# Kernel tuning notes

Measured on AMD Instinct MI355X. Metric: run time of the kernel, lower is better.

## Reference

```python
import jax, jax.numpy as jnp
import numpy as np

B, S, DM, H, DFF, NL = 4, 1024, 512, 8, 2048, 2
D = DM // H
EPS = 1e-9


def setup_inputs() -> dict:
    key = jax.random.key(0)
    ks = jax.random.split(key, 16)
    x = jax.random.normal(ks[0], (B, S, DM), jnp.float32)
    # padding-style mask: 1.0 where attention is blocked
    pad = (jax.random.uniform(ks[1], (B, S)) < 0.1).astype(jnp.float32)
    mask = jnp.maximum(pad[:, :, None], pad[:, None, :])  # [B,S,S]
    protok = jax.random.randint(ks[2], (B, S), 0, 21).astype(jnp.int32)

    def w(k, fan_in, fan_out):
        lim = np.sqrt(6.0 / (fan_in + fan_out)).astype(np.float32)
        return jax.random.uniform(k, (fan_in, fan_out), jnp.float32, -lim, lim)

    return {
        "x": x, "mask": mask, "protok": protok,
        "wq": w(ks[3], DM, DM), "bq": jnp.zeros((DM,), jnp.float32),
        "wk": w(ks[4], DM, DM), "bk": jnp.zeros((DM,), jnp.float32),
        "wv": w(ks[5], DM, DM), "bv": jnp.zeros((DM,), jnp.float32),
        "wo": w(ks[6], DM, DM), "bo": jnp.zeros((DM,), jnp.float32),
        "w1": w(ks[7], DM, DFF), "b1": jnp.zeros((DFF,), jnp.float32),
        "w2": w(ks[8], DFF, DM), "b2": jnp.zeros((DM,), jnp.float32),
        "ln1_g": jnp.ones((DM,), jnp.float32), "ln1_b": jnp.zeros((DM,), jnp.float32),
        "ln2_g": jnp.ones((DM,), jnp.float32), "ln2_b": jnp.zeros((DM,), jnp.float32),
        "layer_num": NL,
    }


def _layernorm(y, g, b):
    m = jnp.mean(y, axis=-1, keepdims=True)
    v = jnp.mean(jnp.square(y - m), axis=-1, keepdims=True)
    return (y - m) * jax.lax.rsqrt(v + EPS) * g + b


def reference(x, mask, protok, wq, bq, wk, bk, wv, bv, wo, bo,
              w1, b1, w2, b2, ln1_g, ln1_b, ln2_g, ln2_b, layer_num):
    b, s, dm = x.shape
    # count_nonzero(protok[0:1,:]) rescale for the 2D softmax (seq == max_pro_len)
    nz = jnp.count_nonzero(protok[0]).astype(jnp.float32)
    neg = mask[:, None, :, :] * -1e9  # [B,1,S,S] broadcast over heads

    def split(t):  # [B,S,DM] -> [B,H,S,D]
        return t.reshape(b, s, H, D).transpose(0, 2, 1, 3)

    def layer(h):
        q = split(h @ wq + bq)
        k = split(h @ wk + bk)
        v = split(h @ wv + bv)
        logits = jnp.einsum('bhid,bhjd->bhij', q, k) / jnp.sqrt(jnp.float32(D))
        logits = logits + neg
        # 2D softmax jointly over axes (2,3), then rescale by nonzero-token count
        A = jax.nn.softmax(logits.reshape(b, H, s * s), axis=-1).reshape(b, H, s, s) * nz
        # faithful quirk: output = A^T @ v
        o = jnp.einsum('bhji,bhjd->bhid', A, v)
        o = o.transpose(0, 2, 1, 3).reshape(b, s, dm)
        attn_out = o @ wo + bo
        out1 = _layernorm(h + attn_out, ln1_g, ln1_b)
        ffn = jax.nn.relu(out1 @ w1 + b1) @ w2 + b2
        return _layernorm(out1 + ffn, ln2_g, ln2_b)

    # Encoders reuses one shared layer layer_num times (self.rencoder overwritten in loop)
    for _ in range(int(layer_num)):
        x = layer(x)
    return x
```

## Files before the change

kernel.cpp:

```cpp
#include <hip/hip_runtime.h>

typedef unsigned short u16;
typedef __bf16 bf16x8 __attribute__((ext_vector_type(8)));
typedef float f32x4 __attribute__((ext_vector_type(4)));
typedef u16 u16x4 __attribute__((ext_vector_type(4)));

#define LOG2E 1.44269504089f
#define SOFF 16.0f

__device__ __forceinline__ f32x4 mfma16(bf16x8 a, bf16x8 b, f32x4 c) {
    return __builtin_amdgcn_mfma_f32_16x16x32_bf16(a, b, c, 0, 0, 0);
}
__device__ __forceinline__ u16 f2bf(float f) {
    union { float f; unsigned u; } x; x.f = f;
    unsigned r = x.u + 0x7FFFu + ((x.u >> 16) & 1u);
    return (u16)(r >> 16);
}
__device__ __forceinline__ float bf2f(u16 u) {
    union { unsigned u; float f; } x; x.u = ((unsigned)u) << 16;
    return x.f;
}
__device__ __forceinline__ void gload_lds16(const u16* g, u16* l) {
    __builtin_amdgcn_global_load_lds((const __attribute__((address_space(1))) unsigned int*)g,
                                     (__attribute__((address_space(3))) unsigned int*)l, 16, 0, 0);
}


__global__ __launch_bounds__(256) void f32_to_bf16_kernel(const float* __restrict__ in, u16* __restrict__ out) {
    const int i = (blockIdx.x * 256 + threadIdx.x) * 8;
    f32x4 a = *(const f32x4*)(in + i);
    f32x4 b = *(const f32x4*)(in + i + 4);
    u16x4 o0, o1;
#pragma unroll
    for (int k = 0; k < 4; ++k) { o0[k] = f2bf(a[k]); o1[k] = f2bf(b[k]); }
    *(u16x4*)(out + i) = o0;
    *(u16x4*)(out + i + 4) = o1;
}

__global__ __launch_bounds__(256) void transpose_f32_bf16(const float* __restrict__ in, u16* __restrict__ out,
                                                          int R, int C) {
    __shared__ float t[32][33];
    const int tx = threadIdx.x & 31, ty = threadIdx.x >> 5;
    const int c0 = blockIdx.x * 32, r0 = blockIdx.y * 32;
#pragma unroll
    for (int k = 0; k < 4; ++k) t[ty + k * 8][tx] = in[(r0 + ty + k * 8) * C + c0 + tx];
    __syncthreads();
#pragma unroll
    for (int k = 0; k < 4; ++k) out[(c0 + ty + k * 8) * R + r0 + tx] = f2bf(t[tx][ty + k * 8]);
}

__global__ __launch_bounds__(256) void transpose4_f32_bf16(
    const float* __restrict__ w0, const float* __restrict__ w1,
    const float* __restrict__ w2, const float* __restrict__ w3,
    u16* __restrict__ o0, u16* __restrict__ o1, u16* __restrict__ o2, u16* __restrict__ o3) {
    __shared__ float t[32][33];
    const int z = blockIdx.z;
    const float* in = z == 0 ? w0 : (z == 1 ? w1 : (z == 2 ? w2 : w3));
    u16* out = z == 0 ? o0 : (z == 1 ? o1 : (z == 2 ? o2 : o3));
    const int tx = threadIdx.x & 31, ty = threadIdx.x >> 5;
    const int c0 = blockIdx.x * 32, r0 = blockIdx.y * 32;
#pragma unroll
    for (int k = 0; k < 4; ++k) t[ty + k * 8][tx] = in[(r0 + ty + k * 8) * 512 + c0 + tx];
    __syncthreads();
#pragma unroll
    for (int k = 0; k < 4; ++k) out[(c0 + ty + k * 8) * 512 + r0 + tx] = f2bf(t[tx][ty + k * 8]);
}

__global__ void count_nz(const int* __restrict__ pk, float* __restrict__ nzf) {
    __shared__ int red[256];
    int c = 0;
    for (int i = threadIdx.x; i < 1024; i += 256) c += (pk[i] != 0) ? 1 : 0;
    red[threadIdx.x] = c;
    __syncthreads();
    for (int s = 128; s > 0; s >>= 1) {
        if (threadIdx.x < s) red[threadIdx.x] += red[threadIdx.x + s];
        __syncthreads();
    }
    if (threadIdx.x == 0) nzf[0] = (float)red[0];
}

__global__ __launch_bounds__(256) void pad_extract(const float* __restrict__ mask, float* __restrict__ padneg) {
    const int i = blockIdx.x * 256 + threadIdx.x;
    const int b = i >> 10, s = i & 1023;
    const float m = mask[((size_t)((b << 10) + s)) * 1024 + s];
    padneg[i] = (m > 0.5f) ? -1.5e9f : -SOFF;
}

template <int BM, int BN, int MODE>
__global__ __launch_bounds__(256) void gemm_bf16(
    const u16* __restrict__ A,
    const u16* __restrict__ Bt0, const u16* __restrict__ Bt1, const u16* __restrict__ Bt2,
    const float* __restrict__ bias0, const float* __restrict__ bias1, const float* __restrict__ bias2,
    void* __restrict__ dst0, void* __restrict__ dst1, void* __restrict__ dst2,
    const int K, const int N) {
    constexpr int BK = 64;
    constexpr int WM = BM / 2, WN = BN / 2, MI = WM / 16, NI = WN / 16;
    __shared__ u16 lA[BM * BK];
    __shared__ u16 lB[BN * BK];
    const int tid = threadIdx.x;
    const int w = tid >> 6, lane = tid & 63, q = lane >> 4, ln = lane & 15;
    const int wm = w >> 1, wn = w & 1;
    const int n0 = blockIdx.x * BN, m0 = blockIdx.y * BM;
    const int rr = lane >> 3;
    const int cs = ((lane & 7) ^ rr) * 8;

    const u16* Bt;
    const float* bias;
    int nb, sel = 0;
    if (MODE == 0) {
        sel = n0 >> 9;
        Bt = sel == 0 ? Bt0 : (sel == 1 ? Bt1 : Bt2);
        bias = sel == 0 ? bias0 : (sel == 1 ? bias1 : bias2);
        nb = n0 & 511;
    } else {
        Bt = Bt0; bias = bias0; nb = n0;
    }
    int kbeg = 0, kend = K;
    if (MODE == 3) { const int kh = K >> 1; kbeg = blockIdx.z * kh; kend = kbeg + kh; }

    const f32x4 vzero = {0.f, 0.f, 0.f, 0.f};
    f32x4 acc[MI][NI];
#pragma unroll
    for (int i = 0; i < MI; ++i)
#pragma unroll
        for (int j = 0; j < NI; ++j) acc[i][j] = vzero;

    const int swa = ln & 7;
    for (int k0 = kbeg; k0 < kend; k0 += BK) {
        const u16* Ag = A + (size_t)m0 * K + k0;
        const u16* Bg = Bt + (size_t)nb * K + k0;
#pragma unroll
        for (int c = 0; c < BM / 32; ++c) {
            const int r = (w * (BM / 32) + c) * 8;
            gload_lds16(Ag + (size_t)(r + rr) * K + cs, &lA[r * BK]);
        }
#pragma unroll
        for (int c = 0; c < BN / 32; ++c) {
            const int r = (w * (BN / 32) + c) * 8;
            gload_lds16(Bg + (size_t)(r + rr) * K + cs, &lB[r * BK]);
        }
        __syncthreads();
#pragma unroll
        for (int kb = 0; kb < 2; ++kb) {
            bf16x8 af[MI], bfr[NI];
#pragma unroll
            for (int mi = 0; mi < MI; ++mi)
                af[mi] = *(const bf16x8*)&lA[(wm * WM + mi * 16 + ln) * BK + ((((kb << 2) + q) ^ swa) << 3)];
#pragma unroll
            for (int ni = 0; ni < NI; ++ni)
                bfr[ni] = *(const bf16x8*)&lB[(wn * WN + ni * 16 + ln) * BK + ((((kb << 2) + q) ^ swa) << 3)];
#pragma unroll
            for (int mi = 0; mi < MI; ++mi)
#pragma unroll
                for (int ni = 0; ni < NI; ++ni) acc[mi][ni] = mfma16(af[mi], bfr[ni], acc[mi][ni]);
        }
        __syncthreads();
    }

    const float scl = (MODE == 0 && sel == 1) ? 0.125f * LOG2E : 1.0f;
#pragma unroll
    for (int mi = 0; mi < MI; ++mi) {
#pragma unroll
        for (int ni = 0; ni < NI; ++ni) {
            const int col = n0 + wn * WN + ni * 16 + ln;
            const float bv = (MODE == 3) ? 0.f : bias[MODE == 0 ? (col & 511) : col];
#pragma unroll
            for (int r = 0; r < 4; ++r) {
                const int row = m0 + wm * WM + mi * 16 + q * 4 + r;
                const float v = (acc[mi][ni][r] + bv) * scl;
                if (MODE == 0) {
                    const int cc = col & 511, hh = cc >> 6, dd = cc & 63;
                    const int bb = row >> 10, ss = row & 1023;
                    if (sel < 2) {
                        u16* dq = (u16*)(sel == 0 ? dst0 : dst1);
                        dq[(((bb << 3) + hh) * 1024 + ss) * 64 + dd] = f2bf(v);
                    } else {
                        ((u16*)dst2)[(((bb << 3) + hh) * 64 + dd) * 1024 + ss] = f2bf(v);
                    }
                } else if (MODE == 1) {
                    ((float*)dst0)[(size_t)row * N + col] = v;
                } else if (MODE == 2) {
                    ((u16*)dst0)[(size_t)row * N + col] = f2bf(fmaxf(v, 0.f));
                } else {
                    float* d = (float*)(blockIdx.z == 0 ? dst0 : dst1);
                    d[(size_t)row * N + col] = v;
                }
            }
        }
    }
}

#define PSTR 68
__global__ __launch_bounds__(256) void flash_kernel(
    const u16* __restrict__ Kb, const u16* __restrict__ Qb, const u16* __restrict__ VT,
    const float* __restrict__ padneg,
    u16* __restrict__ Ounc, float* __restrict__ lrowc) {
    __shared__ u16 ldsQ[64 * 64];
    __shared__ u16 ldsV[64 * 64];
    __shared__ u16 P[4][16 * PSTR];
    const int blk = blockIdx.x, ck = blockIdx.y;
    const int it = blk & 15, bh = blk >> 4, b = bh >> 3;
    const int i0 = it << 6;
    const int tid = threadIdx.x;
    const int w = tid >> 6, lane = tid & 63, q = lane >> 4, ln = lane & 15;

    const u16* Ka = Kb + ((bh << 10) + i0 + (w << 4) + ln) * 64;
    const bf16x8 af0 = *(const bf16x8*)(Ka + q * 8);
    const bf16x8 af1 = *(const bf16x8*)(Ka + 32 + q * 8);
    const u16* Qbase = Qb + (bh << 10) * 64;
    const u16* Vbase = VT + (bh << 6) * 1024;
    const float* pn = padneg + (b << 10);
    float pi[4];
#pragma unroll
    for (int r = 0; r < 4; ++r) pi[r] = pn[i0 + (w << 4) + (q << 2) + r];

    float lsum[4] = {0.f, 0.f, 0.f, 0.f};
    const f32x4 vzero = {0.f, 0.f, 0.f, 0.f};
    f32x4 acc[4] = {vzero, vzero, vzero, vzero};
    u16* Pw = &P[w][0];

    const int srow = lane >> 3;
    const int scol = ((lane & 7) ^ srow) * 8;
    const int sw = ln & 7;
    const int half = w & 1;

    for (int js = 0; js < 4; ++js) {
        const int j0 = (ck << 8) + (js << 6);
        if (w < 2) {
            const u16* src = Qbase + (size_t)(j0 + half * 32) * 64;
#pragma unroll
            for (int c = 0; c < 4; ++c) {
                const int r = half * 32 + c * 8;
                gload_lds16(src + (size_t)(c * 8 + srow) * 64 + scol, &ldsQ[r * 64]);
            }
        } else {
            const u16* src = Vbase + (size_t)(half * 32) * 1024 + j0;
#pragma unroll
            for (int c = 0; c < 4; ++c) {
                const int r = half * 32 + c * 8;
                gload_lds16(src + (size_t)(c * 8 + srow) * 1024 + scol, &ldsV[r * 64]);
            }
        }
        __syncthreads();
#pragma unroll
        for (int jt = 0; jt < 4; ++jt) {
            const int jr = (jt << 4) + ln;
            const float pj = pn[j0 + jr];
            bf16x8 b0 = *(const bf16x8*)&ldsQ[jr * 64 + ((q ^ sw) << 3)];
            bf16x8 b1 = *(const bf16x8*)&ldsQ[jr * 64 + (((q + 4) ^ sw) << 3)];
            f32x4 c = vzero;
            c = mfma16(af0, b0, c);
            c = mfma16(af1, b1, c);
#pragma unroll
            for (int r = 0; r < 4; ++r) {
                const float pe = exp2f(c[r] + fminf(pi[r], pj));
                lsum[r] += pe;
                Pw[((q << 2) + r) * PSTR + (jt << 4) + ln] = f2bf(pe);
            }
        }
        const bf16x8 pa0 = *(const bf16x8*)(Pw + ln * PSTR + q * 8);
        const bf16x8 pa1 = *(const bf16x8*)(Pw + ln * PSTR + 32 + q * 8);
#pragma unroll
        for (int ds = 0; ds < 4; ++ds) {
            const int vr = (ds << 4) + ln;
            bf16x8 v0 = *(const bf16x8*)&ldsV[vr * 64 + ((q ^ sw) << 3)];
            bf16x8 v1 = *(const bf16x8*)&ldsV[vr * 64 + (((q + 4) ^ sw) << 3)];
            acc[ds] = mfma16(pa0, v0, acc[ds]);
            acc[ds] = mfma16(pa1, v1, acc[ds]);
        }
        __syncthreads();
    }
    const int t = (bh << 10) + i0 + (w << 4) + (q << 2);
    u16* Oc = Ounc + ((size_t)ck << 21);
#pragma unroll
    for (int ds = 0; ds < 4; ++ds)
#pragma unroll
        for (int r = 0; r < 4; ++r) Oc[(size_t)(t + r) * 64 + (ds << 4) + ln] = f2bf(acc[ds][r]);
#pragma unroll
    for (int r = 0; r < 4; ++r) {
        float s = lsum[r];
#pragma unroll
        for (int o = 1; o < 16; o <<= 1) s += __shfl_xor(s, o);
        if (ln == 0) lrowc[(ck << 15) + t + r] = s;
    }
}

__global__ __launch_bounds__(256) void combine_z(
    const float* __restrict__ lrowc, const float* __restrict__ nzf, float* __restrict__ Zs) {
    const int bh = blockIdx.x;
    const int tid = threadIdx.x, w = tid >> 6, lane = tid & 63;
    __shared__ float z4[4];
    float z = 0.f;
#pragma unroll
    for (int c = 0; c < 4; ++c)
        for (int i = tid; i < 1024; i += 256) z += lrowc[(c << 15) + (bh << 10) + i];
#pragma unroll
    for (int o = 32; o > 0; o >>= 1) z += __shfl_xor(z, o);
    if (lane == 0) z4[w] = z;
    __syncthreads();
    if (tid == 0) Zs[bh] = nzf[0] / (z4[0] + z4[1] + z4[2] + z4[3]);
}

__global__ __launch_bounds__(256) void scale_o(
    const u16* __restrict__ Ounc, const float* __restrict__ Zs, u16* __restrict__ obf) {
    const int t = blockIdx.x * 4 + (threadIdx.x >> 6);
    const int lane = threadIdx.x & 63;
    const int bh = t >> 10, i = t & 1023, b = bh >> 3, h = bh & 7;
    float v = 0.f;
#pragma unroll
    for (int c = 0; c < 4; ++c) v += bf2f(Ounc[((size_t)c << 21) + (size_t)t * 64 + lane]);
    obf[((b << 10) + i) * 512 + (h << 6) + lane] = f2bf(v * Zs[bh]);
}

template <int ND>
__global__ __launch_bounds__(256) void ln_kernel(
    const float* __restrict__ base, const float* __restrict__ d1, const float* __restrict__ d2,
    const float* __restrict__ cb,
    const float* __restrict__ g, const float* __restrict__ bb,
    float* __restrict__ of32, u16* __restrict__ obf) {
    const int t = blockIdx.x * 4 + (threadIdx.x >> 6);
    const int lane = threadIdx.x & 63;
    const int off = t * 512 + lane * 8;
    f32x4 a0 = *(const f32x4*)(base + off);
    f32x4 a1 = *(const f32x4*)(base + off + 4);
    f32x4 e0 = *(const f32x4*)(d1 + off);
    f32x4 e1 = *(const f32x4*)(d1 + off + 4);
    float v[8];
#pragma unroll
    for (int k = 0; k < 4; ++k) { v[k] = a0[k] + e0[k]; v[k + 4] = a1[k] + e1[k]; }
    if (ND == 2) {
        f32x4 f0 = *(const f32x4*)(d2 + off);
        f32x4 f1v = *(const f32x4*)(d2 + off + 4);
        f32x4 c0 = *(const f32x4*)(cb + lane * 8);
        f32x4 c1 = *(const f32x4*)(cb + lane * 8 + 4);
#pragma unroll
        for (int k = 0; k < 4; ++k) { v[k] += f0[k] + c0[k]; v[k + 4] += f1v[k] + c1[k]; }
    }
    float s = 0.f;
#pragma unroll
    for (int k = 0; k < 8; ++k) s += v[k];
#pragma unroll
    for (int o = 32; o > 0; o >>= 1) s += __shfl_xor(s, o);
    const float mean = s * (1.f / 512.f);
    float vs = 0.f;
#pragma unroll
    for (int k = 0; k < 8; ++k) { const float d = v[k] - mean; vs += d * d; }
#pragma unroll
    for (int o = 32; o > 0; o >>= 1) vs += __shfl_xor(vs, o);
    const float r = rsqrtf(vs * (1.f / 512.f) + 1e-9f);
    f32x4 y0, y1;
    u16x4 o0, o1;
#pragma unroll
    for (int k = 0; k < 4; ++k) {
        const int c = lane * 8 + k;
        const float ya = (v[k] - mean) * r * g[c] + bb[c];
        y0[k] = ya; o0[k] = f2bf(ya);
        const int c2 = c + 4;
        const float yb = (v[k + 4] - mean) * r * g[c2] + bb[c2];
        y1[k] = yb; o1[k] = f2bf(yb);
    }
    *(f32x4*)(of32 + off) = y0;
    *(f32x4*)(of32 + off + 4) = y1;
    *(u16x4*)(obf + off) = o0;
    *(u16x4*)(obf + off + 4) = o1;
}


extern "C" void kernel_launch(void* const* d_in, const int* in_sizes, int n_in,
                              void* d_out, int out_size, void* d_ws, size_t ws_size,
                              hipStream_t stream) {
    const float* x = (const float*)d_in[0];
    const float* mask = (const float*)d_in[1];
    const int* protok = (const int*)d_in[2];
    const float* wq = (const float*)d_in[3]; const float* bq = (const float*)d_in[4];
    const float* wk = (const float*)d_in[5]; const float* bk = (const float*)d_in[6];
    const float* wv = (const float*)d_in[7]; const float* bv = (const float*)d_in[8];
    const float* wo = (const float*)d_in[9]; const float* bo = (const float*)d_in[10];
    const float* w1 = (const float*)d_in[11]; const float* b1 = (const float*)d_in[12];
    const float* w2 = (const float*)d_in[13]; const float* b2 = (const float*)d_in[14];
    const float* ln1g = (const float*)d_in[15]; const float* ln1b = (const float*)d_in[16];
    const float* ln2g = (const float*)d_in[17]; const float* ln2b = (const float*)d_in[18];

    char* p = (char*)d_ws;
    auto take = [&](size_t bytes) -> char* {
        char* r = p;
        p += (bytes + 255) & ~(size_t)255;
        return r;
    };
    u16* wqT = (u16*)take(512 * 512 * 2);
    u16* wkT = (u16*)take(512 * 512 * 2);
    u16* wvT = (u16*)take(512 * 512 * 2);
    u16* woT = (u16*)take(512 * 512 * 2);
    u16* w1T = (u16*)take(2048 * 512 * 2);
    u16* w2T = (u16*)take(512 * 2048 * 2);
    u16* hbf = (u16*)take(4096 * 512 * 2);
    float* hf32 = (float*)take(4096 * 512 * 4);
    u16* qb = (u16*)take(32 * 1024 * 64 * 2);
    u16* kb = (u16*)take(32 * 1024 * 64 * 2);
    u16* vT = (u16*)take(32 * 64 * 1024 * 2);
    u16* Ounc = (u16*)take(4ull * 32 * 1024 * 64 * 2);
    float* lrowc = (float*)take(4 * 32768 * 4);
    float* Zs = (float*)take(64 * 4);
    float* nzf = (float*)take(256);
    float* padneg = (float*)take(4096 * 4);
    u16* obf = (u16*)take(4096 * 512 * 2);
    float* attn = (float*)take(4096 * 512 * 4);
    float* out1f = (float*)take(4096 * 512 * 4);
    u16* out1bf = (u16*)take(4096 * 512 * 2);
    u16* f1 = (u16*)take(4096 * 2048 * 2);
    float* ffn0 = (float*)take(4096 * 512 * 4);
    float* ffn1 = (float*)take(4096 * 512 * 4);

    f32_to_bf16_kernel<<<dim3(1024), 256, 0, stream>>>(x, hbf);
    transpose4_f32_bf16<<<dim3(16, 16, 4), 256, 0, stream>>>(wq, wk, wv, wo, wqT, wkT, wvT, woT);
    transpose_f32_bf16<<<dim3(64, 16), 256, 0, stream>>>(w1, w1T, 512, 2048);
    transpose_f32_bf16<<<dim3(16, 64), 256, 0, stream>>>(w2, w2T, 2048, 512);
    count_nz<<<dim3(1), 256, 0, stream>>>(protok, nzf);
    pad_extract<<<dim3(16), 256, 0, stream>>>(mask, padneg);

    const float* hin = x;
    for (int l = 0; l < 2; ++l) {
        gemm_bf16<128, 64, 0><<<dim3(24, 32), 256, 0, stream>>>(
            hbf, wqT, wkT, wvT, bq, bk, bv, qb, kb, vT, 512, 1536);
        flash_kernel<<<dim3(512, 4), 256, 0, stream>>>(kb, qb, vT, padneg, Ounc, lrowc);
        combine_z<<<dim3(32), 256, 0, stream>>>(lrowc, nzf, Zs);
        scale_o<<<dim3(8192), 256, 0, stream>>>(Ounc, Zs, obf);
        gemm_bf16<64, 64, 1><<<dim3(8, 64), 256, 0, stream>>>(
            obf, woT, woT, woT, bo, bo, bo, attn, attn, attn, 512, 512);
        ln_kernel<1><<<dim3(1024), 256, 0, stream>>>(hin, attn, nullptr, nullptr, ln1g, ln1b, out1f, out1bf);
        gemm_bf16<128, 64, 2><<<dim3(32, 32), 256, 0, stream>>>(
            out1bf, w1T, w1T, w1T, b1, b1, b1, f1, f1, f1, 512, 2048);
        gemm_bf16<128, 64, 3><<<dim3(8, 32, 2), 256, 0, stream>>>(
            f1, w2T, w2T, w2T, b2, b2, b2, ffn0, ffn1, ffn1, 2048, 512);
        float* hout = (l == 1) ? (float*)d_out : hf32;
        ln_kernel<2><<<dim3(1024), 256, 0, stream>>>(out1f, ffn0, ffn1, b2, ln2g, ln2b, hout, hbf);
        hin = hf32;
    }
}
```

Before: 356.8 us.

## Merge prep kernels, atomic Z reduction, drop split-K FFN2, retile FFN1

Six setup launches (bf16 conversion, weight transposes, pad extraction, nonzero count) become one prep kernel. The flash kernel now atomically accumulates per-head softmax sums into Zs, which the QKV GEMM zeroes, so combine_z and the lrowc buffer go away. FFN2 drops split-K and runs as a 64x64 MODE 1 GEMM over the full K, which lets the second layernorm read a single delta. FFN1 moves to 128x128 tiles. Launch count and extra buffers shrink, at the cost of float-atomic nondeterminism and fewer blocks (512) for the long-K FFN2 GEMM.

```diff
diff --git a/kernel.cpp b/kernel.cpp
--- a/kernel.cpp
+++ b/kernel.cpp
@@ -26,64 +26,66 @@
 }
 
 
-__global__ __launch_bounds__(256) void f32_to_bf16_kernel(const float* __restrict__ in, u16* __restrict__ out) {
-    const int i = (blockIdx.x * 256 + threadIdx.x) * 8;
-    f32x4 a = *(const f32x4*)(in + i);
-    f32x4 b = *(const f32x4*)(in + i + 4);
-    u16x4 o0, o1;
-#pragma unroll
-    for (int k = 0; k < 4; ++k) { o0[k] = f2bf(a[k]); o1[k] = f2bf(b[k]); }
-    *(u16x4*)(out + i) = o0;
-    *(u16x4*)(out + i + 4) = o1;
-}
-
-__global__ __launch_bounds__(256) void transpose_f32_bf16(const float* __restrict__ in, u16* __restrict__ out,
-                                                          int R, int C) {
+__device__ __forceinline__ void transp_tile(const float* __restrict__ in, u16* __restrict__ out,
+                                            int R, int C, int r0, int c0,
+                                            float (*t)[33], int tid) {
+    const int tx = tid & 31, ty = tid >> 5;
+#pragma unroll
+    for (int k = 0; k < 4; ++k) t[ty + k * 8][tx] = in[(size_t)(r0 + ty + k * 8) * C + c0 + tx];
+    __syncthreads();
+#pragma unroll
+    for (int k = 0; k < 4; ++k) out[(size_t)(c0 + ty + k * 8) * R + r0 + tx] = f2bf(t[tx][ty + k * 8]);
+}
+
+__global__ __launch_bounds__(256) void prep_kernel(
+    const float* __restrict__ x,
+    const float* __restrict__ wq, const float* __restrict__ wk,
+    const float* __restrict__ wv, const float* __restrict__ wo,
+    const float* __restrict__ w1, const float* __restrict__ w2,
+    const float* __restrict__ mask, const int* __restrict__ protok,
+    u16* __restrict__ hbf, u16* __restrict__ wqT, u16* __restrict__ wkT,
+    u16* __restrict__ wvT, u16* __restrict__ woT, u16* __restrict__ w1T, u16* __restrict__ w2T,
+    float* __restrict__ padneg, float* __restrict__ nzf) {
     __shared__ float t[32][33];
-    const int tx = threadIdx.x & 31, ty = threadIdx.x >> 5;
-    const int c0 = blockIdx.x * 32, r0 = blockIdx.y * 32;
-#pragma unroll
-    for (int k = 0; k < 4; ++k) t[ty + k * 8][tx] = in[(r0 + ty + k * 8) * C + c0 + tx];
-    __syncthreads();
-#pragma unroll
-    for (int k = 0; k < 4; ++k) out[(c0 + ty + k * 8) * R + r0 + tx] = f2bf(t[tx][ty + k * 8]);
-}
-
-__global__ __launch_bounds__(256) void transpose4_f32_bf16(
-    const float* __restrict__ w0, const float* __restrict__ w1,
-    const float* __restrict__ w2, const float* __restrict__ w3,
-    u16* __restrict__ o0, u16* __restrict__ o1, u16* __restrict__ o2, u16* __restrict__ o3) {
-    __shared__ float t[32][33];
-    const int z = blockIdx.z;
-    const float* in = z == 0 ? w0 : (z == 1 ? w1 : (z == 2 ? w2 : w3));
-    u16* out = z == 0 ? o0 : (z == 1 ? o1 : (z == 2 ? o2 : o3));
-    const int tx = threadIdx.x & 31, ty = threadIdx.x >> 5;
-    const int c0 = blockIdx.x * 32, r0 = blockIdx.y * 32;
-#pragma unroll
-    for (int k = 0; k < 4; ++k) t[ty + k * 8][tx] = in[(r0 + ty + k * 8) * 512 + c0 + tx];
-    __syncthreads();
-#pragma unroll
-    for (int k = 0; k < 4; ++k) out[(c0 + ty + k * 8) * 512 + r0 + tx] = f2bf(t[tx][ty + k * 8]);
-}
-
-__global__ void count_nz(const int* __restrict__ pk, float* __restrict__ nzf) {
     __shared__ int red[256];
-    int c = 0;
-    for (int i = threadIdx.x; i < 1024; i += 256) c += (pk[i] != 0) ? 1 : 0;
-    red[threadIdx.x] = c;
-    __syncthreads();
-    for (int s = 128; s > 0; s >>= 1) {
-        if (threadIdx.x < s) red[threadIdx.x] += red[threadIdx.x + s];
+    const int id = blockIdx.x, tid = threadIdx.x;
+    if (id < 1024) {
+        const int z = id >> 8, rem = id & 255;
+        const float* in = z == 0 ? wq : (z == 1 ? wk : (z == 2 ? wv : wo));
+        u16* out = z == 0 ? wqT : (z == 1 ? wkT : (z == 2 ? wvT : woT));
+        transp_tile(in, out, 512, 512, (rem >> 4) * 32, (rem & 15) * 32, t, tid);
+    } else if (id < 2048) {
+        const int rem = id - 1024;
+        transp_tile(w1, w1T, 512, 2048, (rem >> 6) * 32, (rem & 63) * 32, t, tid);
+    } else if (id < 3072) {
+        const int rem = id - 2048;
+        transp_tile(w2, w2T, 2048, 512, (rem >> 4) * 32, (rem & 15) * 32, t, tid);
+    } else if (id < 4096) {
+        const int i = ((id - 3072) * 256 + tid) * 8;
+        f32x4 a = *(const f32x4*)(x + i);
+        f32x4 b = *(const f32x4*)(x + i + 4);
+        u16x4 o0, o1;
+#pragma unroll
+        for (int k = 0; k < 4; ++k) { o0[k] = f2bf(a[k]); o1[k] = f2bf(b[k]); }
+        *(u16x4*)(hbf + i) = o0;
+        *(u16x4*)(hbf + i + 4) = o1;
+    } else if (id == 4096) {
+        for (int i = tid; i < 4096; i += 256) {
+            const int b = i >> 10, s = i & 1023;
+            const float m = mask[(size_t)((b << 10) + s) * 1024 + s];
+            padneg[i] = (m > 0.5f) ? -1.5e9f : -SOFF;
+        }
+    } else {
+        int c = 0;
+        for (int i = tid; i < 1024; i += 256) c += (protok[i] != 0) ? 1 : 0;
+        red[tid] = c;
         __syncthreads();
-    }
-    if (threadIdx.x == 0) nzf[0] = (float)red[0];
-}
-
-__global__ __launch_bounds__(256) void pad_extract(const float* __restrict__ mask, float* __restrict__ padneg) {
-    const int i = blockIdx.x * 256 + threadIdx.x;
-    const int b = i >> 10, s = i & 1023;
-    const float m = mask[((size_t)((b << 10) + s)) * 1024 + s];
-    padneg[i] = (m > 0.5f) ? -1.5e9f : -SOFF;
+        for (int s = 128; s > 0; s >>= 1) {
+            if (tid < s) red[tid] += red[tid + s];
+            __syncthreads();
+        }
+        if (tid == 0) nzf[0] = (float)red[0];
+    }
 }
 
 template <int BM, int BN, int MODE>
@@ -92,6 +94,7 @@
     const u16* __restrict__ Bt0, const u16* __restrict__ Bt1, const u16* __restrict__ Bt2,
     const float* __restrict__ bias0, const float* __restrict__ bias1, const float* __restrict__ bias2,
     void* __restrict__ dst0, void* __restrict__ dst1, void* __restrict__ dst2,
+    float* __restrict__ Zs,
     const int K, const int N) {
     constexpr int BK = 64;
     constexpr int WM = BM / 2, WN = BN / 2, MI = WM / 16, NI = WN / 16;
@@ -104,6 +107,8 @@
     const int rr = lane >> 3;
     const int cs = ((lane & 7) ^ rr) * 8;
 
+    if (MODE == 0 && blockIdx.x == 0 && blockIdx.y == 0 && tid < 32) Zs[tid] = 0.f;
+
     const u16* Bt;
     const float* bias;
     int nb, sel = 0;
@@ -115,8 +120,6 @@
     } else {
         Bt = Bt0; bias = bias0; nb = n0;
     }
-    int kbeg = 0, kend = K;
-    if (MODE == 3) { const int kh = K >> 1; kbeg = blockIdx.z * kh; kend = kbeg + kh; }
 
     const f32x4 vzero = {0.f, 0.f, 0.f, 0.f};
     f32x4 acc[MI][NI];
@@ -126,7 +129,7 @@
         for (int j = 0; j < NI; ++j) acc[i][j] = vzero;
 
     const int swa = ln & 7;
-    for (int k0 = kbeg; k0 < kend; k0 += BK) {
+    for (int k0 = 0; k0 < K; k0 += BK) {
         const u16* Ag = A + (size_t)m0 * K + k0;
         const u16* Bg = Bt + (size_t)nb * K + k0;
 #pragma unroll
@@ -163,7 +166,7 @@
 #pragma unroll
         for (int ni = 0; ni < NI; ++ni) {
             const int col = n0 + wn * WN + ni * 16 + ln;
-            const float bv = (MODE == 3) ? 0.f : bias[MODE == 0 ? (col & 511) : col];
+            const float bv = bias[MODE == 0 ? (col & 511) : col];
 #pragma unroll
             for (int r = 0; r < 4; ++r) {
                 const int row = m0 + wm * WM + mi * 16 + q * 4 + r;
@@ -179,11 +182,8 @@
                     }
                 } else if (MODE == 1) {
                     ((float*)dst0)[(size_t)row * N + col] = v;
-                } else if (MODE == 2) {
+                } else {
                     ((u16*)dst0)[(size_t)row * N + col] = f2bf(fmaxf(v, 0.f));
-                } else {
-                    float* d = (float*)(blockIdx.z == 0 ? dst0 : dst1);
-                    d[(size_t)row * N + col] = v;
                 }
             }
         }
@@ -194,7 +194,7 @@
 __global__ __launch_bounds__(256) void flash_kernel(
     const u16* __restrict__ Kb, const u16* __restrict__ Qb, const u16* __restrict__ VT,
     const float* __restrict__ padneg,
-    u16* __restrict__ Ounc, float* __restrict__ lrowc) {
+    u16* __restrict__ Ounc, float* __restrict__ Zs) {
     __shared__ u16 ldsQ[64 * 64];
     __shared__ u16 ldsV[64 * 64];
     __shared__ u16 P[4][16 * PSTR];
@@ -276,46 +276,27 @@
     for (int ds = 0; ds < 4; ++ds)
 #pragma unroll
         for (int r = 0; r < 4; ++r) Oc[(size_t)(t + r) * 64 + (ds << 4) + ln] = f2bf(acc[ds][r]);
-#pragma unroll
-    for (int r = 0; r < 4; ++r) {
-        float s = lsum[r];
-#pragma unroll
-        for (int o = 1; o < 16; o <<= 1) s += __shfl_xor(s, o);
-        if (ln == 0) lrowc[(ck << 15) + t + r] = s;
-    }
-}
-
-__global__ __launch_bounds__(256) void combine_z(
-    const float* __restrict__ lrowc, const float* __restrict__ nzf, float* __restrict__ Zs) {
-    const int bh = blockIdx.x;
-    const int tid = threadIdx.x, w = tid >> 6, lane = tid & 63;
-    __shared__ float z4[4];
-    float z = 0.f;
-#pragma unroll
-    for (int c = 0; c < 4; ++c)
-        for (int i = tid; i < 1024; i += 256) z += lrowc[(c << 15) + (bh << 10) + i];
-#pragma unroll
-    for (int o = 32; o > 0; o >>= 1) z += __shfl_xor(z, o);
-    if (lane == 0) z4[w] = z;
-    __syncthreads();
-    if (tid == 0) Zs[bh] = nzf[0] / (z4[0] + z4[1] + z4[2] + z4[3]);
+    float s = (lsum[0] + lsum[1]) + (lsum[2] + lsum[3]);
+#pragma unroll
+    for (int o = 1; o < 64; o <<= 1) s += __shfl_xor(s, o);
+    if (lane == 0) atomicAdd(&Zs[bh], s);
 }
 
 __global__ __launch_bounds__(256) void scale_o(
-    const u16* __restrict__ Ounc, const float* __restrict__ Zs, u16* __restrict__ obf) {
+    const u16* __restrict__ Ounc, const float* __restrict__ Zs, const float* __restrict__ nzf,
+    u16* __restrict__ obf) {
     const int t = blockIdx.x * 4 + (threadIdx.x >> 6);
     const int lane = threadIdx.x & 63;
     const int bh = t >> 10, i = t & 1023, b = bh >> 3, h = bh & 7;
+    const float fac = nzf[0] / Zs[bh];
     float v = 0.f;
 #pragma unroll
     for (int c = 0; c < 4; ++c) v += bf2f(Ounc[((size_t)c << 21) + (size_t)t * 64 + lane]);
-    obf[((b << 10) + i) * 512 + (h << 6) + lane] = f2bf(v * Zs[bh]);
-}
-
-template <int ND>
+    obf[((b << 10) + i) * 512 + (h << 6) + lane] = f2bf(v * fac);
+}
+
 __global__ __launch_bounds__(256) void ln_kernel(
-    const float* __restrict__ base, const float* __restrict__ d1, const float* __restrict__ d2,
-    const float* __restrict__ cb,
+    const float* __restrict__ base, const float* __restrict__ delta,
     const float* __restrict__ g, const float* __restrict__ bb,
     float* __restrict__ of32, u16* __restrict__ obf) {
     const int t = blockIdx.x * 4 + (threadIdx.x >> 6);
@@ -323,19 +304,11 @@
     const int off = t * 512 + lane * 8;
     f32x4 a0 = *(const f32x4*)(base + off);
     f32x4 a1 = *(const f32x4*)(base + off + 4);
-    f32x4 e0 = *(const f32x4*)(d1 + off);
-    f32x4 e1 = *(const f32x4*)(d1 + off + 4);
+    f32x4 e0 = *(const f32x4*)(delta + off);
+    f32x4 e1 = *(const f32x4*)(delta + off + 4);
     float v[8];
 #pragma unroll
     for (int k = 0; k < 4; ++k) { v[k] = a0[k] + e0[k]; v[k + 4] = a1[k] + e1[k]; }
-    if (ND == 2) {
-        f32x4 f0 = *(const f32x4*)(d2 + off);
-        f32x4 f1v = *(const f32x4*)(d2 + off + 4);
-        f32x4 c0 = *(const f32x4*)(cb + lane * 8);
-        f32x4 c1 = *(const f32x4*)(cb + lane * 8 + 4);
-#pragma unroll
-        for (int k = 0; k < 4; ++k) { v[k] += f0[k] + c0[k]; v[k + 4] += f1v[k] + c1[k]; }
-    }
     float s = 0.f;
 #pragma unroll
     for (int k = 0; k < 8; ++k) s += v[k];
@@ -399,7 +372,6 @@
     u16* kb = (u16*)take(32 * 1024 * 64 * 2);
     u16* vT = (u16*)take(32 * 64 * 1024 * 2);
     u16* Ounc = (u16*)take(4ull * 32 * 1024 * 64 * 2);
-    float* lrowc = (float*)take(4 * 32768 * 4);
     float* Zs = (float*)take(64 * 4);
     float* nzf = (float*)take(256);
     float* padneg = (float*)take(4096 * 4);
@@ -408,32 +380,27 @@
     float* out1f = (float*)take(4096 * 512 * 4);
     u16* out1bf = (u16*)take(4096 * 512 * 2);
     u16* f1 = (u16*)take(4096 * 2048 * 2);
-    float* ffn0 = (float*)take(4096 * 512 * 4);
-    float* ffn1 = (float*)take(4096 * 512 * 4);
-
-    f32_to_bf16_kernel<<<dim3(1024), 256, 0, stream>>>(x, hbf);
-    transpose4_f32_bf16<<<dim3(16, 16, 4), 256, 0, stream>>>(wq, wk, wv, wo, wqT, wkT, wvT, woT);
-    transpose_f32_bf16<<<dim3(64, 16), 256, 0, stream>>>(w1, w1T, 512, 2048);
-    transpose_f32_bf16<<<dim3(16, 64), 256, 0, stream>>>(w2, w2T, 2048, 512);
-    count_nz<<<dim3(1), 256, 0, stream>>>(protok, nzf);
-    pad_extract<<<dim3(16), 256, 0, stream>>>(mask, padneg);
+    float* ffn = attn;
+
+    prep_kernel<<<dim3(4098), 256, 0, stream>>>(
+        x, wq, wk, wv, wo, w1, w2, mask, protok,
+        hbf, wqT, wkT, wvT, woT, w1T, w2T, padneg, nzf);
 
     const float* hin = x;
     for (int l = 0; l < 2; ++l) {
         gemm_bf16<128, 64, 0><<<dim3(24, 32), 256, 0, stream>>>(
-            hbf, wqT, wkT, wvT, bq, bk, bv, qb, kb, vT, 512, 1536);
-        flash_kernel<<<dim3(512, 4), 256, 0, stream>>>(kb, qb, vT, padneg, Ounc, lrowc);
-        combine_z<<<dim3(32), 256, 0, stream>>>(lrowc, nzf, Zs);
-        scale_o<<<dim3(8192), 256, 0, stream>>>(Ounc, Zs, obf);
+            hbf, wqT, wkT, wvT, bq, bk, bv, qb, kb, vT, Zs, 512, 1536);
+        flash_kernel<<<dim3(512, 4), 256, 0, stream>>>(kb, qb, vT, padneg, Ounc, Zs);
+        scale_o<<<dim3(8192), 256, 0, stream>>>(Ounc, Zs, nzf, obf);
         gemm_bf16<64, 64, 1><<<dim3(8, 64), 256, 0, stream>>>(
-            obf, woT, woT, woT, bo, bo, bo, attn, attn, attn, 512, 512);
-        ln_kernel<1><<<dim3(1024), 256, 0, stream>>>(hin, attn, nullptr, nullptr, ln1g, ln1b, out1f, out1bf);
-        gemm_bf16<128, 64, 2><<<dim3(32, 32), 256, 0, stream>>>(
-            out1bf, w1T, w1T, w1T, b1, b1, b1, f1, f1, f1, 512, 2048);
-        gemm_bf16<128, 64, 3><<<dim3(8, 32, 2), 256, 0, stream>>>(
-            f1, w2T, w2T, w2T, b2, b2, b2, ffn0, ffn1, ffn1, 2048, 512);
+            obf, woT, woT, woT, bo, bo, bo, attn, attn, attn, nullptr, 512, 512);
+        ln_kernel<<<dim3(1024), 256, 0, stream>>>(hin, attn, ln1g, ln1b, out1f, out1bf);
+        gemm_bf16<128, 128, 2><<<dim3(16, 32), 256, 0, stream>>>(
+            out1bf, w1T, w1T, w1T, b1, b1, b1, f1, f1, f1, nullptr, 512, 2048);
+        gemm_bf16<64, 64, 1><<<dim3(8, 64), 256, 0, stream>>>(
+            f1, w2T, w2T, w2T, b2, b2, b2, ffn, ffn, ffn, nullptr, 2048, 512);
         float* hout = (l == 1) ? (float*)d_out : hf32;
-        ln_kernel<2><<<dim3(1024), 256, 0, stream>>>(out1f, ffn0, ffn1, b2, ln2g, ln2b, hout, hbf);
+        ln_kernel<<<dim3(1024), 256, 0, stream>>>(out1f, ffn, ln2g, ln2b, hout, hbf);
         hin = hf32;
     }
 }
```

After: 432.6 us. 1.21x slower.
